# Optimization experiments

Hardware: AMD Instinct MI355X
Metric: run time of the kernel (lower is better)

The kernel has to match this reference:

```python
import jax, jax.numpy as jnp
import numpy as np

B, S, D, H = 2, 2048, 1024, 16
HD = D // H  # head_dim = 64


def setup_inputs() -> dict:
    key = jax.random.key(0)
    k1, k2, k3 = jax.random.split(key, 3)
    x = jax.random.normal(k1, (B, S, D), dtype=jnp.float32)
    W_attn = jax.random.normal(k2, (3 * D, D), dtype=jnp.float32) * (D ** -0.5)
    W_proj = jax.random.normal(k3, (D, D), dtype=jnp.float32) * (D ** -0.5)
    b_proj = jnp.zeros((D,), dtype=jnp.float32)
    return {"x": x, "W_attn": W_attn, "W_proj": W_proj, "b_proj": b_proj}


def reference(x, W_attn, W_proj, b_proj):
    b, s, d = x.shape
    h, hd = H, d // H
    # fused QKV projection (torch Linear: x @ W^T), then split
    qkv = jnp.einsum('bsd,ed->bse', x, W_attn)  # [B,S,3D]
    q, k, v = jnp.split(qkv, 3, axis=-1)
    # [B,S,D] -> [B,H,S,hd]
    q = q.reshape(b, s, h, hd).transpose(0, 2, 1, 3)
    k = k.reshape(b, s, h, hd).transpose(0, 2, 1, 3)
    v = v.reshape(b, s, h, hd).transpose(0, 2, 1, 3)
    # manual softmax attention (no causal mask in the non-flash branch)
    att = jnp.einsum('bhqd,bhkd->bhqk', q, k) * (1.0 / jnp.sqrt(jnp.float32(hd)))
    att = jax.nn.softmax(att, axis=-1)  # attn_dropout is identity in eval
    y = jnp.einsum('bhqk,bhkd->bhqd', att, v)
    y = y.transpose(0, 2, 1, 3).reshape(b, s, d)
    y = jnp.einsum('bsd,ed->bse', y, W_proj) + b_proj  # resid_dropout identity
    return y, att
```

## Files before the change

kernel.cpp:

```cpp
#include <hip/hip_runtime.h>

typedef _Float16 f16;
typedef f16 f16x4 __attribute__((ext_vector_type(4)));
typedef f16 f16x8 __attribute__((ext_vector_type(8)));
typedef float f32x4 __attribute__((ext_vector_type(4)));
typedef unsigned int u32;
typedef unsigned long long u64;

#define DEV static __device__ __forceinline__

#define S_ 2048
#define D_ 1024

#define S_WAITV(n) asm volatile("s_waitcnt vmcnt(" #n ") lgkmcnt(0)" ::: "memory")

DEV int swz64(int row, int chunk) { return row * 64 + (((chunk ^ row) & 7) << 3); }

DEV void gload16(const void* g, void* l) {
    __builtin_amdgcn_global_load_lds((const __attribute__((address_space(1))) u32*)g,
                                     (__attribute__((address_space(3))) u32*)l, 16, 0, 0);
}
DEV float exp2_fast(float x) { float r; asm("v_exp_f32 %0, %1" : "=v"(r) : "v"(x)); return r; }
DEV void nt_store4(float* p, f32x4 v) { __builtin_nontemporal_store(v, (f32x4*)p); }

__global__ void convert_f16(const float* __restrict__ x, const float* __restrict__ wa,
                            const float* __restrict__ wp,
                            f16* __restrict__ xb, f16* __restrict__ wab, f16* __restrict__ wpb) {
    u32 t = blockIdx.x * blockDim.x + threadIdx.x;
    u32 base = t * 8u;
    const float* src; f16* dst; u32 off;
    if (base < 4194304u)      { src = x;  dst = xb;  off = base; }
    else if (base < 7340032u) { src = wa; dst = wab; off = base - 4194304u; }
    else                      { src = wp; dst = wpb; off = base - 7340032u; }
    float4 a = *(const float4*)(src + off);
    float4 b = *(const float4*)(src + off + 4);
    f16x8 v;
    v[0] = (f16)a.x; v[1] = (f16)a.y; v[2] = (f16)a.z; v[3] = (f16)a.w;
    v[4] = (f16)b.x; v[5] = (f16)b.y; v[6] = (f16)b.z; v[7] = (f16)b.w;
    *(f16x8*)(dst + off) = v;
}

template <int EPI>
__global__ __launch_bounds__(256) void gemm_bt(
    const f16* __restrict__ A, const f16* __restrict__ Bt, int K,
    f16* __restrict__ oQ, f16* __restrict__ oK, f16* __restrict__ oV,
    float* __restrict__ oY, const float* __restrict__ bias) {
    __shared__ f16 smem[3][8192];
    f16* sm = &smem[0][0];
    const int tid = threadIdx.x;
    const int lane = tid & 63;
    const int la = lane & 15, lg = lane >> 4;
    const int wv = tid >> 6;
    const int wr = (wv >> 1) << 6, wc = (wv & 1) << 6;
    const int r0 = blockIdx.x << 7, c0 = blockIdx.y << 7;

    const f32x4 VZ = {0.f, 0.f, 0.f, 0.f};
    f32x4 acc[4][4];
#pragma unroll
    for (int m = 0; m < 4; ++m)
#pragma unroll
        for (int n = 0; n < 4; ++n) acc[m][n] = VZ;

    const int srow = tid >> 2, scol = (tid & 3) << 3;
    const f16* Ag = A + (u64)(r0 + srow) * K + scol;
    const f16* Bg = Bt + (u64)(c0 + srow) * K + scol;
    const u64 K64 = (u64)K << 6;

    const int NT = K >> 5;
#define STAGE(k0, slot)                                              \
    do {                                                             \
        f16* Al = smem[slot] + wv * 512;                             \
        f16* Bl = smem[slot] + 4096 + wv * 512;                      \
        gload16(Ag + (k0), Al);                                      \
        gload16(Ag + K64 + (k0), Al + 2048);                         \
        gload16(Bg + (k0), Bl);                                      \
        gload16(Bg + K64 + (k0), Bl + 2048);                         \
    } while (0)

    STAGE(0, 0);
    STAGE(32, 1);
    S_WAITV(4);
    __builtin_amdgcn_s_barrier();

    for (int t = 0; t < NT; ++t) {
        if (t > 0) {
            if (t < NT - 1) { S_WAITV(4); } else { S_WAITV(0); }
            __builtin_amdgcn_s_barrier();
        }
        if (t + 2 < NT) STAGE((t + 2) << 5, (t + 2) % 3);
        const f16* As = smem[t % 3];
        const f16* Bs = smem[t % 3] + 4096;
        f16x8 af[4], bf[4];
#pragma unroll
        for (int m = 0; m < 4; ++m) af[m] = *(const f16x8*)(As + (wr + m * 16 + la) * 32 + lg * 8);
#pragma unroll
        for (int n = 0; n < 4; ++n) bf[n] = *(const f16x8*)(Bs + (wc + n * 16 + la) * 32 + lg * 8);
#pragma unroll
        for (int m = 0; m < 4; ++m)
#pragma unroll
            for (int n = 0; n < 4; ++n)
                acc[m][n] = __builtin_amdgcn_mfma_f32_16x16x32_f16(af[m], bf[n], acc[m][n], 0, 0, 0);
    }
#undef STAGE

    if (EPI == 0) {
        if (c0 < 2048) {
#pragma unroll
            for (int n = 0; n < 4; ++n) {
                int col = c0 + wc + n * 16 + la;
#pragma unroll
                for (int m = 0; m < 4; ++m) {
#pragma unroll
                    for (int j = 0; j < 4; ++j) {
                        int row = r0 + wr + m * 16 + lg * 4 + j;
                        int b = row >> 11, s = row & 2047;
                        float val = acc[m][n][j];
                        if (col < 1024) {
                            int h = col >> 6, hd = col & 63;
                            oQ[(((u64)(b * 16 + h)) * 2048 + s) * 64 + hd] = (f16)(val * 0.18033688f);
                        } else {
                            int d = col - 1024, h = d >> 6, hd = d & 63;
                            oK[(((u64)(b * 16 + h)) * 2048 + s) * 64 + hd] = (f16)val;
                        }
                    }
                }
            }
        } else {
            const int hbase = (c0 - 2048) >> 6;
            const int b = r0 >> 11, sb = r0 & 2047;
#pragma unroll
            for (int hh = 0; hh < 2; ++hh) {
                __syncthreads();
                if ((wv & 1) == hh) {
#pragma unroll
                    for (int n = 0; n < 4; ++n) {
                        int hd = n * 16 + la;
#pragma unroll
                        for (int m = 0; m < 4; ++m) {
                            int s = wr + m * 16 + lg * 4;
                            int pos = (s & ~31) | (lg << 3) | (((s >> 4) & 1) << 2);
                            f16x4 pk;
                            pk[0] = (f16)acc[m][n][0]; pk[1] = (f16)acc[m][n][1];
                            pk[2] = (f16)acc[m][n][2]; pk[3] = (f16)acc[m][n][3];
                            *(f16x4*)(sm + hd * 136 + pos) = pk;
                        }
                    }
                }
                __syncthreads();
                {
                    int hd = tid >> 2, qtr = tid & 3;
                    f16* dst = oV + (((u64)(b * 16 + hbase + hh)) * 64 + hd) * 2048 + sb + qtr * 32;
#pragma unroll
                    for (int i = 0; i < 4; ++i)
                        *(f16x8*)(dst + i * 8) = *(const f16x8*)(sm + hd * 136 + qtr * 32 + i * 8);
                }
            }
        }
    } else {
#pragma unroll
        for (int n = 0; n < 4; ++n) {
            int col = c0 + wc + n * 16 + la;
            float bv = bias[col];
#pragma unroll
            for (int m = 0; m < 4; ++m)
#pragma unroll
                for (int j = 0; j < 4; ++j) {
                    int row = r0 + wr + m * 16 + lg * 4 + j;
                    oY[(u64)row * 1024 + col] = acc[m][n][j] + bv;
                }
        }
    }
}

__global__ __launch_bounds__(256) void attn_fused(
    const f16* __restrict__ q, const f16* __restrict__ k, const f16* __restrict__ vt,
    float* __restrict__ att, f16* __restrict__ ya) {
    __shared__ f16 smem[25088];
    f16* qs = smem + 4 * 4096;

    const int tid = threadIdx.x, lane = tid & 63, wv = tid >> 6;
    const int la = lane & 15, lg = lane >> 4;
    const int bh = blockIdx.x, qt = blockIdx.y;
    const f16* qh = q + (u64)bh * (S_ * 64) + qt * (64 * 64);
    const f16* kh = k + (u64)bh * (S_ * 64);
    const f16* vh = vt + (u64)bh * (S_ * 64);

    char* const Pw = (char*)smem + 32768 + wv * 4352;

    const int sr0 = wv * 8 + (lane >> 3);
    const int sr1 = sr0 + 32;
    const int sc0 = (((lane & 7) ^ (sr0 & 7)) << 3);
    const int sc1 = (((lane & 7) ^ (sr1 & 7)) << 3);
    const u64 go0 = (u64)sr0 * 64 + sc0, go1 = (u64)sr1 * 64 + sc1;
    const u64 gv0 = (u64)sr0 * 2048 + sc0, gv1 = (u64)sr1 * 2048 + sc1;

    gload16(qh + go0, qs + wv * 512);
    gload16(qh + go1, qs + 2048 + wv * 512);
    gload16(kh + go0, smem + wv * 512);
    gload16(kh + go1, smem + 2048 + wv * 512);
    gload16(kh + 4096 + go0, smem + 4096 + wv * 512);
    gload16(kh + 4096 + go1, smem + 4096 + 2048 + wv * 512);
    S_WAITV(2);
    __builtin_amdgcn_s_barrier();

    f16x8 qf[2];
    qf[0] = *(const f16x8*)(qs + swz64(wv * 16 + la, lg));
    qf[1] = *(const f16x8*)(qs + swz64(wv * 16 + la, 4 + lg));

    const f32x4 VZ = {0.f, 0.f, 0.f, 0.f};
    float psum = 0.f;

    for (int kt = 0; kt < 32; ++kt) {
        if (kt > 0) {
            if (kt < 31) { S_WAITV(2); } else { S_WAITV(0); }
            __builtin_amdgcn_s_barrier();
        }
        if (kt < 30) {
            const f16* kb = kh + (kt + 2) * 4096;
            f16* dst = smem + ((kt + 2) % 3) * 4096;
            gload16(kb + go0, dst + wv * 512);
            gload16(kb + go1, dst + 2048 + wv * 512);
        }
        const f16* kcur = smem + (kt % 3) * 4096;
        f32x4 sc[4] = {VZ, VZ, VZ, VZ};
#pragma unroll
        for (int ch = 0; ch < 2; ++ch)
#pragma unroll
            for (int n = 0; n < 4; ++n) {
                f16x8 kf = *(const f16x8*)(kcur + swz64(n * 16 + la, ch * 4 + lg));
                sc[n] = __builtin_amdgcn_mfma_f32_16x16x32_f16(kf, qf[ch], sc[n], 0, 0, 0);
            }
#pragma unroll
        for (int n = 0; n < 4; ++n)
#pragma unroll
            for (int j = 0; j < 4; ++j) psum += exp2_fast(sc[n][j]);
    }
    S_WAITV(0);
    __builtin_amdgcn_s_barrier();

    psum += __shfl_xor(psum, 16);
    psum += __shfl_xor(psum, 32);
    const float invl = 1.0f / psum;

    gload16(kh + go0, smem + wv * 512);
    gload16(kh + go1, smem + 2048 + wv * 512);
    gload16(vh + gv0, smem + 2 * 4096 + wv * 512);
    gload16(vh + gv1, smem + 2 * 4096 + 2048 + wv * 512);
    S_WAITV(0);
    __builtin_amdgcn_s_barrier();

    f32x4 accy[4] = {VZ, VZ, VZ, VZ};
    float* abw = att + ((u64)bh * S_ + (u64)qt * 64 + wv * 16) * S_;
    for (int kt = 0; kt < 32; ++kt) {
        if (kt > 0) {
            S_WAITV(4);
            __builtin_amdgcn_s_barrier();
        }
        if (kt < 31) {
            const f16* kb = kh + (kt + 1) * 4096;
            const f16* vb = vh + (kt + 1) * 64;
            f16* kd = smem + ((kt + 1) & 1) * 4096;
            f16* vd = smem + (2 + ((kt + 1) & 1)) * 4096;
            gload16(kb + go0, kd + wv * 512);
            gload16(kb + go1, kd + 2048 + wv * 512);
            gload16(vb + gv0, vd + wv * 512);
            gload16(vb + gv1, vd + 2048 + wv * 512);
        }
        const f16* kcur = smem + (kt & 1) * 4096;
        const f16* vcur = smem + (2 + (kt & 1)) * 4096;

        f32x4 sc[4] = {VZ, VZ, VZ, VZ};
#pragma unroll
        for (int ch = 0; ch < 2; ++ch)
#pragma unroll
            for (int n = 0; n < 4; ++n) {
                f16x8 kf = *(const f16x8*)(kcur + swz64(n * 16 + la, ch * 4 + lg));
                sc[n] = __builtin_amdgcn_mfma_f32_16x16x32_f16(kf, qf[ch], sc[n], 0, 0, 0);
            }
        f32x4 pp[4];
#pragma unroll
        for (int n = 0; n < 4; ++n) {
#pragma unroll
            for (int j = 0; j < 4; ++j) pp[n][j] = exp2_fast(sc[n][j]) * invl;
            *(f32x4*)(Pw + la * 272 + n * 64 + lg * 16) = pp[n];
        }
        f16x8 pa0, pa1;
#pragma unroll
        for (int j = 0; j < 4; ++j) {
            pa0[j] = (f16)pp[0][j]; pa0[j + 4] = (f16)pp[1][j];
            pa1[j] = (f16)pp[2][j]; pa1[j + 4] = (f16)pp[3][j];
        }
#pragma unroll
        for (int n = 0; n < 4; ++n) {
            f16x8 vf0 = *(const f16x8*)(vcur + swz64(n * 16 + la, lg));
            accy[n] = __builtin_amdgcn_mfma_f32_16x16x32_f16(pa0, vf0, accy[n], 0, 0, 0);
            f16x8 vf1 = *(const f16x8*)(vcur + swz64(n * 16 + la, 4 + lg));
            accy[n] = __builtin_amdgcn_mfma_f32_16x16x32_f16(pa1, vf1, accy[n], 0, 0, 0);
        }
#pragma unroll
        for (int r = 0; r < 4; ++r) {
            int row = r * 4 + (lane >> 4);
            f32x4 v = *(const f32x4*)(Pw + row * 272 + (lane & 15) * 16);
            nt_store4(abw + (u64)row * S_ + kt * 64 + (lane & 15) * 4, v);
        }
    }

    const int b = bh >> 4, h = bh & 15;
    f16* yb = ya + ((u64)b * S_ + qt * 64 + wv * 16) * D_ + h * 64;
#pragma unroll
    for (int n = 0; n < 4; ++n)
#pragma unroll
        for (int j = 0; j < 4; ++j)
            yb[(u64)(lg * 4 + j) * D_ + n * 16 + la] = (f16)accy[n][j];
}

extern "C" void kernel_launch(void* const* d_in, const int* in_sizes, int n_in,
                              void* d_out, int out_size, void* d_ws, size_t ws_size,
                              hipStream_t stream) {
    const float* x  = (const float*)d_in[0];
    const float* wa = (const float*)d_in[1];
    const float* wp = (const float*)d_in[2];
    const float* bp = (const float*)d_in[3];
    float* outY   = (float*)d_out;
    float* outAtt = outY + 4194304ull;

    char* ws = (char*)d_ws;
    f16* xb  = (f16*)(ws + 0);
    f16* wab = (f16*)(ws + 8388608);
    f16* wpb = (f16*)(ws + 14680064);
    f16* qb  = (f16*)(ws + 16777216);
    f16* kb  = (f16*)(ws + 25165824);
    f16* vtb = (f16*)(ws + 33554432);
    f16* yab = (f16*)(ws + 41943040);

    convert_f16<<<4096, 256, 0, stream>>>(x, wa, wp, xb, wab, wpb);
    gemm_bt<0><<<dim3(32, 24), 256, 0, stream>>>(xb, wab, 1024, qb, kb, vtb, nullptr, nullptr);
    attn_fused<<<dim3(32, 32), 256, 0, stream>>>(qb, kb, vtb, outAtt, yab);
    gemm_bt<1><<<dim3(32, 8), 256, 0, stream>>>(yab, wpb, 1024, nullptr, nullptr, nullptr, outY, bp);
}
```

Before: 227.9 us.

## Split softmax row-sum pass into separate kernel processing two query tiles per block

Moves the first pass of the two-pass softmax (computing exp sums over all keys) out of attn_fused into a new row_sums kernel. Each row_sums block handles 128 query rows, so every K tile loaded into shared memory serves two query tiles and the K reads of this pass are halved. attn_fused now reads the precomputed inverse sums and runs only the second pass. This adds a kernel launch and a small global round trip for the sums, and reuses the start of the xb workspace region, which is safe only because xb is no longer needed once the QKV GEMM has run.

```diff
diff --git a/kernel.cpp b/kernel.cpp
--- a/kernel.cpp
+++ b/kernel.cpp
@@ -172,9 +172,84 @@
     }
 }
 
+__global__ __launch_bounds__(256) void row_sums(
+    const f16* __restrict__ q, const f16* __restrict__ k, float* __restrict__ invl) {
+    __shared__ f16 smem[20480];
+    f16* const QS = smem + 12288;
+    const int tid = threadIdx.x, lane = tid & 63, wv = tid >> 6;
+    const int la = lane & 15, lg = lane >> 4;
+    const int bh = blockIdx.x, qc = blockIdx.y;
+    const f16* qh = q + (u64)bh * (S_ * 64) + qc * (128 * 64);
+    const f16* kh = k + (u64)bh * (S_ * 64);
+
+    const int sr0 = wv * 8 + (lane >> 3);
+    const int sr1 = sr0 + 32;
+    const int sc0 = (((lane & 7) ^ (sr0 & 7)) << 3);
+    const int sc1 = (((lane & 7) ^ (sr1 & 7)) << 3);
+    const u64 go0 = (u64)sr0 * 64 + sc0, go1 = (u64)sr1 * 64 + sc1;
+
+    gload16(qh + go0, QS + wv * 512);
+    gload16(qh + go1, QS + 2048 + wv * 512);
+    gload16(qh + 4096 + go0, QS + 4096 + wv * 512);
+    gload16(qh + 4096 + go1, QS + 4096 + 2048 + wv * 512);
+    gload16(kh + go0, smem + wv * 512);
+    gload16(kh + go1, smem + 2048 + wv * 512);
+    gload16(kh + 4096 + go0, smem + 4096 + wv * 512);
+    gload16(kh + 4096 + go1, smem + 4096 + 2048 + wv * 512);
+    S_WAITV(2);
+    __builtin_amdgcn_s_barrier();
+
+    f16x8 qf[2][2];
+    qf[0][0] = *(const f16x8*)(QS + swz64(wv * 16 + la, lg));
+    qf[0][1] = *(const f16x8*)(QS + swz64(wv * 16 + la, 4 + lg));
+    qf[1][0] = *(const f16x8*)(QS + 4096 + swz64(wv * 16 + la, lg));
+    qf[1][1] = *(const f16x8*)(QS + 4096 + swz64(wv * 16 + la, 4 + lg));
+
+    const f32x4 VZ = {0.f, 0.f, 0.f, 0.f};
+    float psum[2] = {0.f, 0.f};
+
+    for (int kt = 0; kt < 32; ++kt) {
+        if (kt > 0) {
+            if (kt < 31) { S_WAITV(2); } else { S_WAITV(0); }
+            __builtin_amdgcn_s_barrier();
+        }
+        if (kt < 30) {
+            const f16* kb = kh + (kt + 2) * 4096;
+            f16* dst = smem + ((kt + 2) % 3) * 4096;
+            gload16(kb + go0, dst + wv * 512);
+            gload16(kb + go1, dst + 2048 + wv * 512);
+        }
+        const f16* kcur = smem + (kt % 3) * 4096;
+        f32x4 sc[2][4] = {{VZ, VZ, VZ, VZ}, {VZ, VZ, VZ, VZ}};
+#pragma unroll
+        for (int ch = 0; ch < 2; ++ch)
+#pragma unroll
+            for (int n = 0; n < 4; ++n) {
+                f16x8 kf = *(const f16x8*)(kcur + swz64(n * 16 + la, ch * 4 + lg));
+                sc[0][n] = __builtin_amdgcn_mfma_f32_16x16x32_f16(kf, qf[0][ch], sc[0][n], 0, 0, 0);
+                sc[1][n] = __builtin_amdgcn_mfma_f32_16x16x32_f16(kf, qf[1][ch], sc[1][n], 0, 0, 0);
+            }
+#pragma unroll
+        for (int s = 0; s < 2; ++s)
+#pragma unroll
+            for (int n = 0; n < 4; ++n)
+#pragma unroll
+                for (int j = 0; j < 4; ++j) psum[s] += exp2_fast(sc[s][n][j]);
+    }
+
+#pragma unroll
+    for (int s = 0; s < 2; ++s) {
+        float t = psum[s];
+        t += __shfl_xor(t, 16);
+        t += __shfl_xor(t, 32);
+        if (lg == 0)
+            invl[(u64)bh * S_ + qc * 128 + s * 64 + wv * 16 + la] = 1.0f / t;
+    }
+}
+
 __global__ __launch_bounds__(256) void attn_fused(
     const f16* __restrict__ q, const f16* __restrict__ k, const f16* __restrict__ vt,
-    float* __restrict__ att, f16* __restrict__ ya) {
+    const float* __restrict__ sums, float* __restrict__ att, f16* __restrict__ ya) {
     __shared__ f16 smem[25088];
     f16* qs = smem + 4 * 4096;
 
@@ -194,60 +269,23 @@
     const u64 go0 = (u64)sr0 * 64 + sc0, go1 = (u64)sr1 * 64 + sc1;
     const u64 gv0 = (u64)sr0 * 2048 + sc0, gv1 = (u64)sr1 * 2048 + sc1;
 
+    const float invl = sums[(u64)bh * S_ + qt * 64 + wv * 16 + la];
+    asm volatile("" :: "v"(invl));
+
     gload16(qh + go0, qs + wv * 512);
     gload16(qh + go1, qs + 2048 + wv * 512);
-    gload16(kh + go0, smem + wv * 512);
-    gload16(kh + go1, smem + 2048 + wv * 512);
-    gload16(kh + 4096 + go0, smem + 4096 + wv * 512);
-    gload16(kh + 4096 + go1, smem + 4096 + 2048 + wv * 512);
-    S_WAITV(2);
-    __builtin_amdgcn_s_barrier();
-
-    f16x8 qf[2];
-    qf[0] = *(const f16x8*)(qs + swz64(wv * 16 + la, lg));
-    qf[1] = *(const f16x8*)(qs + swz64(wv * 16 + la, 4 + lg));
-
-    const f32x4 VZ = {0.f, 0.f, 0.f, 0.f};
-    float psum = 0.f;
-
-    for (int kt = 0; kt < 32; ++kt) {
-        if (kt > 0) {
-            if (kt < 31) { S_WAITV(2); } else { S_WAITV(0); }
-            __builtin_amdgcn_s_barrier();
-        }
-        if (kt < 30) {
-            const f16* kb = kh + (kt + 2) * 4096;
-            f16* dst = smem + ((kt + 2) % 3) * 4096;
-            gload16(kb + go0, dst + wv * 512);
-            gload16(kb + go1, dst + 2048 + wv * 512);
-        }
-        const f16* kcur = smem + (kt % 3) * 4096;
-        f32x4 sc[4] = {VZ, VZ, VZ, VZ};
-#pragma unroll
-        for (int ch = 0; ch < 2; ++ch)
-#pragma unroll
-            for (int n = 0; n < 4; ++n) {
-                f16x8 kf = *(const f16x8*)(kcur + swz64(n * 16 + la, ch * 4 + lg));
-                sc[n] = __builtin_amdgcn_mfma_f32_16x16x32_f16(kf, qf[ch], sc[n], 0, 0, 0);
-            }
-#pragma unroll
-        for (int n = 0; n < 4; ++n)
-#pragma unroll
-            for (int j = 0; j < 4; ++j) psum += exp2_fast(sc[n][j]);
-    }
-    S_WAITV(0);
-    __builtin_amdgcn_s_barrier();
-
-    psum += __shfl_xor(psum, 16);
-    psum += __shfl_xor(psum, 32);
-    const float invl = 1.0f / psum;
-
     gload16(kh + go0, smem + wv * 512);
     gload16(kh + go1, smem + 2048 + wv * 512);
     gload16(vh + gv0, smem + 2 * 4096 + wv * 512);
     gload16(vh + gv1, smem + 2 * 4096 + 2048 + wv * 512);
     S_WAITV(0);
     __builtin_amdgcn_s_barrier();
+
+    f16x8 qf[2];
+    qf[0] = *(const f16x8*)(qs + swz64(wv * 16 + la, lg));
+    qf[1] = *(const f16x8*)(qs + swz64(wv * 16 + la, 4 + lg));
+
+    const f32x4 VZ = {0.f, 0.f, 0.f, 0.f};
 
     f32x4 accy[4] = {VZ, VZ, VZ, VZ};
     float* abw = att + ((u64)bh * S_ + (u64)qt * 64 + wv * 16) * S_;
@@ -332,9 +370,11 @@
     f16* kb  = (f16*)(ws + 25165824);
     f16* vtb = (f16*)(ws + 33554432);
     f16* yab = (f16*)(ws + 41943040);
+    float* il = (float*)(ws + 0);
 
     convert_f16<<<4096, 256, 0, stream>>>(x, wa, wp, xb, wab, wpb);
     gemm_bt<0><<<dim3(32, 24), 256, 0, stream>>>(xb, wab, 1024, qb, kb, vtb, nullptr, nullptr);
-    attn_fused<<<dim3(32, 32), 256, 0, stream>>>(qb, kb, vtb, outAtt, yab);
+    row_sums<<<dim3(32, 16), 256, 0, stream>>>(qb, kb, il);
+    attn_fused<<<dim3(32, 32), 256, 0, stream>>>(qb, kb, vtb, il, outAtt, yab);
     gemm_bt<1><<<dim3(32, 8), 256, 0, stream>>>(yab, wpb, 1024, nullptr, nullptr, nullptr, outY, bp);
 }
```

Measured after the change: 237.8 us. 1.04x slower.

## Process 128 query rows per attention block to halve K/V reloads

Applied to the files above, without the earlier changes.

Each attention block now handles two 64-row query sub-tiles instead of one, so every K and V tile loaded into shared memory is reused for twice as many queries. The grid's query dimension is halved to match. This cuts global K/V traffic and per-block setup overhead. In exchange it adds register pressure from the doubled accumulators and query fragments, launches fewer blocks (512), and the Q staging buffer now shares space with the P scratch area.

```diff
diff --git a/kernel.cpp b/kernel.cpp
--- a/kernel.cpp
+++ b/kernel.cpp
@@ -176,16 +176,16 @@
     const f16* __restrict__ q, const f16* __restrict__ k, const f16* __restrict__ vt,
     float* __restrict__ att, f16* __restrict__ ya) {
     __shared__ f16 smem[25088];
-    f16* qs = smem + 4 * 4096;
+    f16* const PQ = smem + 16384;
 
     const int tid = threadIdx.x, lane = tid & 63, wv = tid >> 6;
     const int la = lane & 15, lg = lane >> 4;
     const int bh = blockIdx.x, qt = blockIdx.y;
-    const f16* qh = q + (u64)bh * (S_ * 64) + qt * (64 * 64);
+    const f16* qh = q + (u64)bh * (S_ * 64) + qt * (128 * 64);
     const f16* kh = k + (u64)bh * (S_ * 64);
     const f16* vh = vt + (u64)bh * (S_ * 64);
 
-    char* const Pw = (char*)smem + 32768 + wv * 4352;
+    char* const Pw = (char*)PQ + wv * 4352;
 
     const int sr0 = wv * 8 + (lane >> 3);
     const int sr1 = sr0 + 32;
@@ -194,21 +194,30 @@
     const u64 go0 = (u64)sr0 * 64 + sc0, go1 = (u64)sr1 * 64 + sc1;
     const u64 gv0 = (u64)sr0 * 2048 + sc0, gv1 = (u64)sr1 * 2048 + sc1;
 
-    gload16(qh + go0, qs + wv * 512);
-    gload16(qh + go1, qs + 2048 + wv * 512);
     gload16(kh + go0, smem + wv * 512);
     gload16(kh + go1, smem + 2048 + wv * 512);
     gload16(kh + 4096 + go0, smem + 4096 + wv * 512);
     gload16(kh + 4096 + go1, smem + 4096 + 2048 + wv * 512);
-    S_WAITV(2);
-    __builtin_amdgcn_s_barrier();
-
-    f16x8 qf[2];
-    qf[0] = *(const f16x8*)(qs + swz64(wv * 16 + la, lg));
-    qf[1] = *(const f16x8*)(qs + swz64(wv * 16 + la, 4 + lg));
+    gload16(qh + go0, PQ + wv * 512);
+    gload16(qh + go1, PQ + 2048 + wv * 512);
+    S_WAITV(0);
+    __builtin_amdgcn_s_barrier();
+
+    f16x8 qf[2][2];
+    qf[0][0] = *(const f16x8*)(PQ + swz64(wv * 16 + la, lg));
+    qf[0][1] = *(const f16x8*)(PQ + swz64(wv * 16 + la, 4 + lg));
+    asm volatile("s_waitcnt lgkmcnt(0)" ::: "memory");
+    __builtin_amdgcn_s_barrier();
+
+    gload16(qh + 4096 + go0, PQ + wv * 512);
+    gload16(qh + 4096 + go1, PQ + 2048 + wv * 512);
+    S_WAITV(0);
+    __builtin_amdgcn_s_barrier();
+    qf[1][0] = *(const f16x8*)(PQ + swz64(wv * 16 + la, lg));
+    qf[1][1] = *(const f16x8*)(PQ + swz64(wv * 16 + la, 4 + lg));
 
     const f32x4 VZ = {0.f, 0.f, 0.f, 0.f};
-    float psum = 0.f;
+    float psum[2] = {0.f, 0.f};
 
     for (int kt = 0; kt < 32; ++kt) {
         if (kt > 0) {
@@ -222,25 +231,33 @@
             gload16(kb + go1, dst + 2048 + wv * 512);
         }
         const f16* kcur = smem + (kt % 3) * 4096;
-        f32x4 sc[4] = {VZ, VZ, VZ, VZ};
+        f32x4 sc[2][4] = {{VZ, VZ, VZ, VZ}, {VZ, VZ, VZ, VZ}};
 #pragma unroll
         for (int ch = 0; ch < 2; ++ch)
 #pragma unroll
             for (int n = 0; n < 4; ++n) {
                 f16x8 kf = *(const f16x8*)(kcur + swz64(n * 16 + la, ch * 4 + lg));
-                sc[n] = __builtin_amdgcn_mfma_f32_16x16x32_f16(kf, qf[ch], sc[n], 0, 0, 0);
-            }
-#pragma unroll
-        for (int n = 0; n < 4; ++n)
-#pragma unroll
-            for (int j = 0; j < 4; ++j) psum += exp2_fast(sc[n][j]);
+                sc[0][n] = __builtin_amdgcn_mfma_f32_16x16x32_f16(kf, qf[0][ch], sc[0][n], 0, 0, 0);
+                sc[1][n] = __builtin_amdgcn_mfma_f32_16x16x32_f16(kf, qf[1][ch], sc[1][n], 0, 0, 0);
+            }
+#pragma unroll
+        for (int s = 0; s < 2; ++s)
+#pragma unroll
+            for (int n = 0; n < 4; ++n)
+#pragma unroll
+                for (int j = 0; j < 4; ++j) psum[s] += exp2_fast(sc[s][n][j]);
     }
     S_WAITV(0);
     __builtin_amdgcn_s_barrier();
 
-    psum += __shfl_xor(psum, 16);
-    psum += __shfl_xor(psum, 32);
-    const float invl = 1.0f / psum;
+    float invl[2];
+#pragma unroll
+    for (int s = 0; s < 2; ++s) {
+        float t = psum[s];
+        t += __shfl_xor(t, 16);
+        t += __shfl_xor(t, 32);
+        invl[s] = 1.0f / t;
+    }
 
     gload16(kh + go0, smem + wv * 512);
     gload16(kh + go1, smem + 2048 + wv * 512);
@@ -249,11 +266,11 @@
     S_WAITV(0);
     __builtin_amdgcn_s_barrier();
 
-    f32x4 accy[4] = {VZ, VZ, VZ, VZ};
-    float* abw = att + ((u64)bh * S_ + (u64)qt * 64 + wv * 16) * S_;
+    f32x4 accy[2][4] = {{VZ, VZ, VZ, VZ}, {VZ, VZ, VZ, VZ}};
+    float* abw = att + ((u64)bh * S_ + (u64)qt * 128 + wv * 16) * S_;
     for (int kt = 0; kt < 32; ++kt) {
         if (kt > 0) {
-            S_WAITV(4);
+            S_WAITV(8);
             __builtin_amdgcn_s_barrier();
         }
         if (kt < 31) {
@@ -265,53 +282,61 @@
             gload16(kb + go1, kd + 2048 + wv * 512);
             gload16(vb + gv0, vd + wv * 512);
             gload16(vb + gv1, vd + 2048 + wv * 512);
+            __builtin_amdgcn_sched_barrier(0);
         }
         const f16* kcur = smem + (kt & 1) * 4096;
         const f16* vcur = smem + (2 + (kt & 1)) * 4096;
 
-        f32x4 sc[4] = {VZ, VZ, VZ, VZ};
-#pragma unroll
-        for (int ch = 0; ch < 2; ++ch)
+#pragma unroll
+        for (int qs = 0; qs < 2; ++qs) {
+            f32x4 sc[4] = {VZ, VZ, VZ, VZ};
+#pragma unroll
+            for (int ch = 0; ch < 2; ++ch)
+#pragma unroll
+                for (int n = 0; n < 4; ++n) {
+                    f16x8 kf = *(const f16x8*)(kcur + swz64(n * 16 + la, ch * 4 + lg));
+                    sc[n] = __builtin_amdgcn_mfma_f32_16x16x32_f16(kf, qf[qs][ch], sc[n], 0, 0, 0);
+                }
+            f32x4 pp[4];
 #pragma unroll
             for (int n = 0; n < 4; ++n) {
-                f16x8 kf = *(const f16x8*)(kcur + swz64(n * 16 + la, ch * 4 + lg));
-                sc[n] = __builtin_amdgcn_mfma_f32_16x16x32_f16(kf, qf[ch], sc[n], 0, 0, 0);
-            }
-        f32x4 pp[4];
-#pragma unroll
-        for (int n = 0; n < 4; ++n) {
-#pragma unroll
-            for (int j = 0; j < 4; ++j) pp[n][j] = exp2_fast(sc[n][j]) * invl;
-            *(f32x4*)(Pw + la * 272 + n * 64 + lg * 16) = pp[n];
-        }
-        f16x8 pa0, pa1;
-#pragma unroll
-        for (int j = 0; j < 4; ++j) {
-            pa0[j] = (f16)pp[0][j]; pa0[j + 4] = (f16)pp[1][j];
-            pa1[j] = (f16)pp[2][j]; pa1[j + 4] = (f16)pp[3][j];
-        }
-#pragma unroll
-        for (int n = 0; n < 4; ++n) {
-            f16x8 vf0 = *(const f16x8*)(vcur + swz64(n * 16 + la, lg));
-            accy[n] = __builtin_amdgcn_mfma_f32_16x16x32_f16(pa0, vf0, accy[n], 0, 0, 0);
-            f16x8 vf1 = *(const f16x8*)(vcur + swz64(n * 16 + la, 4 + lg));
-            accy[n] = __builtin_amdgcn_mfma_f32_16x16x32_f16(pa1, vf1, accy[n], 0, 0, 0);
-        }
-#pragma unroll
-        for (int r = 0; r < 4; ++r) {
-            int row = r * 4 + (lane >> 4);
-            f32x4 v = *(const f32x4*)(Pw + row * 272 + (lane & 15) * 16);
-            nt_store4(abw + (u64)row * S_ + kt * 64 + (lane & 15) * 4, v);
+#pragma unroll
+                for (int j = 0; j < 4; ++j) pp[n][j] = exp2_fast(sc[n][j]) * invl[qs];
+                *(f32x4*)(Pw + la * 272 + n * 64 + lg * 16) = pp[n];
+            }
+            f16x8 pa0, pa1;
+#pragma unroll
+            for (int j = 0; j < 4; ++j) {
+                pa0[j] = (f16)pp[0][j]; pa0[j + 4] = (f16)pp[1][j];
+                pa1[j] = (f16)pp[2][j]; pa1[j + 4] = (f16)pp[3][j];
+            }
+#pragma unroll
+            for (int n = 0; n < 4; ++n) {
+                f16x8 vf0 = *(const f16x8*)(vcur + swz64(n * 16 + la, lg));
+                accy[qs][n] = __builtin_amdgcn_mfma_f32_16x16x32_f16(pa0, vf0, accy[qs][n], 0, 0, 0);
+                f16x8 vf1 = *(const f16x8*)(vcur + swz64(n * 16 + la, 4 + lg));
+                accy[qs][n] = __builtin_amdgcn_mfma_f32_16x16x32_f16(pa1, vf1, accy[qs][n], 0, 0, 0);
+            }
+            float* abs_ = abw + (u64)(qs * 64) * S_;
+#pragma unroll
+            for (int r = 0; r < 4; ++r) {
+                int row = r * 4 + (lane >> 4);
+                f32x4 v = *(const f32x4*)(Pw + row * 272 + (lane & 15) * 16);
+                nt_store4(abs_ + (u64)row * S_ + kt * 64 + (lane & 15) * 4, v);
+            }
         }
     }
 
     const int b = bh >> 4, h = bh & 15;
-    f16* yb = ya + ((u64)b * S_ + qt * 64 + wv * 16) * D_ + h * 64;
-#pragma unroll
-    for (int n = 0; n < 4; ++n)
-#pragma unroll
-        for (int j = 0; j < 4; ++j)
-            yb[(u64)(lg * 4 + j) * D_ + n * 16 + la] = (f16)accy[n][j];
+#pragma unroll
+    for (int qs = 0; qs < 2; ++qs) {
+        f16* yb = ya + ((u64)b * S_ + qt * 128 + qs * 64 + wv * 16) * D_ + h * 64;
+#pragma unroll
+        for (int n = 0; n < 4; ++n)
+#pragma unroll
+            for (int j = 0; j < 4; ++j)
+                yb[(u64)(lg * 4 + j) * D_ + n * 16 + la] = (f16)accy[qs][n][j];
+    }
 }
 
 extern "C" void kernel_launch(void* const* d_in, const int* in_sizes, int n_in,
@@ -335,6 +360,6 @@
 
     convert_f16<<<4096, 256, 0, stream>>>(x, wa, wp, xb, wab, wpb);
     gemm_bt<0><<<dim3(32, 24), 256, 0, stream>>>(xb, wab, 1024, qb, kb, vtb, nullptr, nullptr);
-    attn_fused<<<dim3(32, 32), 256, 0, stream>>>(qb, kb, vtb, outAtt, yab);
+    attn_fused<<<dim3(32, 16), 256, 0, stream>>>(qb, kb, vtb, outAtt, yab);
     gemm_bt<1><<<dim3(32, 8), 256, 0, stream>>>(yab, wpb, 1024, nullptr, nullptr, nullptr, outY, bp);
 }
```

Result: slower. 253.3 us (+11.1%).
